# Optimization experiments

Hardware: AMD Instinct MI355X
Metric: run time of the kernel (lower is better)

The kernel has to match this reference:

```python
import jax, jax.numpy as jnp
import numpy as np

N_NODES = 50000
N_EDGES = 800000
N_GRAPHS = 256
F_IN = 128
H = 64
N_CLASSES = 10


def setup_inputs() -> dict:
    key = jax.random.key(0)
    ks = jax.random.split(key, 12)
    x = jax.random.normal(ks[0], (N_NODES, F_IN), dtype=jnp.float32)
    edge_index = jax.random.randint(ks[1], (2, N_EDGES), 0, N_NODES, dtype=jnp.int64)
    batch = jnp.sort(jax.random.randint(ks[2], (N_NODES,), 0, N_GRAPHS, dtype=jnp.int64))
    def glorot(k, fan_in, fan_out):
        lim = np.sqrt(6.0 / (fan_in + fan_out)).astype(np.float32)
        return jax.random.uniform(k, (fan_in, fan_out), jnp.float32, -lim, lim)
    return {
        "x": x,
        "edge_index": edge_index,
        "batch": batch,
        "W1": glorot(ks[3], F_IN, H), "b1": jnp.zeros((H,), jnp.float32),
        "W2": glorot(ks[4], H, H),    "b2": jnp.zeros((H,), jnp.float32),
        "W3": glorot(ks[5], H, H),    "b3": jnp.zeros((H,), jnp.float32),
        "Wm": glorot(ks[6], H, N_CLASSES), "bm": jnp.zeros((N_CLASSES,), jnp.float32),
    }


def _gcn_norm(edge_index, n_nodes):
    # Add self-loops, unit edge weights, symmetric normalization (PyG gcn_norm).
    loops = jnp.arange(n_nodes, dtype=edge_index.dtype)
    row = jnp.concatenate([edge_index[0], loops])  # source
    col = jnp.concatenate([edge_index[1], loops])  # target (aggregation index)
    deg = jax.ops.segment_sum(jnp.ones_like(col, dtype=jnp.float32), col,
                              num_segments=n_nodes)
    dinv = jnp.where(deg > 0, jax.lax.rsqrt(deg), 0.0)
    norm = dinv[row] * dinv[col]  # [E + N]
    return row, col, norm


def _gcn_conv(x, row, col, norm, W, b, n_nodes):
    h = x @ W                                   # [N, H] dense transform
    msg = h[row] * norm[:, None]                # gather + scale  [E+N, H]
    out = jax.ops.segment_sum(msg, col, num_segments=n_nodes)  # scatter-add
    return out + b


def _l2_normalize(x, eps=1e-12):
    n = jnp.sqrt(jnp.sum(x * x, axis=-1, keepdims=True))
    return x / jnp.maximum(n, eps)


def reference(x, edge_index, batch, W1, b1, W2, b2, W3, b3, Wm, bm):
    n = x.shape[0]
    row, col, norm = _gcn_norm(edge_index, n)
    h = x
    for (W, b) in ((W1, b1), (W2, b2), (W3, b3)):
        h = _gcn_conv(h, row, col, norm, W, b, n)
        h = _l2_normalize(h)       # emb_normalize
        h = jax.nn.relu(h)         # gnn_non_linear
    node_emb = h
    # global_mean_pool over graphs
    sums = jax.ops.segment_sum(h, batch, num_segments=N_GRAPHS)
    counts = jax.ops.segment_sum(jnp.ones((n,), jnp.float32), batch,
                                 num_segments=N_GRAPHS)
    graph_emb = sums / jnp.maximum(counts, 1.0)[:, None]
    logits = graph_emb @ Wm + bm
    probs = jax.nn.softmax(logits, axis=-1)
    return logits, probs, node_emb, graph_emb
```

## Files before the change

### kernel.cpp

```cpp
#include <hip/hip_runtime.h>
#include <math.h>

#define HH 64


__global__ void k_init(int* __restrict__ head, float* __restrict__ sums,
                       int* __restrict__ cursor, int n, int pn) {
    int i = blockIdx.x * blockDim.x + threadIdx.x;
    if (i < n) head[i] = -1;
    if (i < pn) sums[i] = 0.f;
    if (i == 0) *cursor = 0;
}

template<int FIN>
__global__ __launch_bounds__(256, 4) void k_link_gemm(const int* __restrict__ col, int E,
                                                      int* __restrict__ head, int* __restrict__ next,
                                                      const float* __restrict__ x,
                                                      const float* __restrict__ W,
                                                      float* __restrict__ lin, int n) {
    constexpr int KC = 32;
    constexpr int XS = 68;
    __shared__ __align__(16) float Ws[FIN][HH];
    __shared__ __align__(16) float xs_t[KC][XS];
    const int tid = threadIdx.x;

    int e0 = blockIdx.x * 1024 + tid;
#pragma unroll
    for (int k = 0; k < 4; ++k) {
        int e = e0 + k * 256;
        if (e < E) {
            int c = col[e];
            int prev = atomicExch(&head[c], e);
            next[e] = prev;
        }
    }

    const int tx = tid & 15;
    const int ty = tid >> 4;
    const int node0 = blockIdx.x * 64;
    if (node0 >= n) return;

    for (int i = tid * 4; i < FIN * HH; i += 1024)
        *(float4*)&Ws[0][i] = *(const float4*)&W[i];

    float acc[4][4] = {};
    const int rr0 = tid >> 3;
    const int cc  = (tid & 7) * 4;

    for (int kc = 0; kc < FIN; kc += KC) {
        __syncthreads();
        for (int rr = rr0; rr < 64; rr += 32) {
            float4 v = make_float4(0.f, 0.f, 0.f, 0.f);
            if (node0 + rr < n) v = *(const float4*)&x[(size_t)(node0 + rr) * FIN + kc + cc];
            xs_t[cc + 0][rr] = v.x;
            xs_t[cc + 1][rr] = v.y;
            xs_t[cc + 2][rr] = v.z;
            xs_t[cc + 3][rr] = v.w;
        }
        __syncthreads();
#pragma unroll 4
        for (int k = 0; k < KC; ++k) {
            float4 a4 = *(const float4*)&xs_t[k][ty * 4];
            float4 b4 = *(const float4*)&Ws[kc + k][tx * 4];
            acc[0][0] = fmaf(a4.x, b4.x, acc[0][0]);
            acc[0][1] = fmaf(a4.x, b4.y, acc[0][1]);
            acc[0][2] = fmaf(a4.x, b4.z, acc[0][2]);
            acc[0][3] = fmaf(a4.x, b4.w, acc[0][3]);
            acc[1][0] = fmaf(a4.y, b4.x, acc[1][0]);
            acc[1][1] = fmaf(a4.y, b4.y, acc[1][1]);
            acc[1][2] = fmaf(a4.y, b4.z, acc[1][2]);
            acc[1][3] = fmaf(a4.y, b4.w, acc[1][3]);
            acc[2][0] = fmaf(a4.z, b4.x, acc[2][0]);
            acc[2][1] = fmaf(a4.z, b4.y, acc[2][1]);
            acc[2][2] = fmaf(a4.z, b4.z, acc[2][2]);
            acc[2][3] = fmaf(a4.z, b4.w, acc[2][3]);
            acc[3][0] = fmaf(a4.w, b4.x, acc[3][0]);
            acc[3][1] = fmaf(a4.w, b4.y, acc[3][1]);
            acc[3][2] = fmaf(a4.w, b4.z, acc[3][2]);
            acc[3][3] = fmaf(a4.w, b4.w, acc[3][3]);
        }
    }

#pragma unroll
    for (int i = 0; i < 4; ++i) {
        int node = node0 + ty * 4 + i;
        if (node < n) *(float4*)&lin[(size_t)node * HH + tx * 4] = *(float4*)acc[i];
    }
}

__global__ __launch_bounds__(256) void k_walk_alloc(const int* __restrict__ row,
                                                    const int* __restrict__ head,
                                                    const int* __restrict__ next,
                                                    int* __restrict__ cursor,
                                                    int* __restrict__ rowptr,
                                                    int* __restrict__ cnt,
                                                    float* __restrict__ dinv,
                                                    int* __restrict__ csr, int n) {
    int node = blockIdx.x * blockDim.x + threadIdx.x;
    int lane = threadIdx.x & 63;
    int len = 0;
    int h = -1;
    if (node < n) {
        h = head[node];
        for (int p = h; p >= 0; p = next[p]) ++len;
        dinv[node] = rsqrtf((float)(len + 1));
    }
    int incl = len;
#pragma unroll
    for (int off = 1; off < 64; off <<= 1) {
        int t = __shfl_up(incl, off, 64);
        if (lane >= off) incl += t;
    }
    int total = __shfl(incl, 63, 64);
    int base = 0;
    if (lane == 0 && total > 0) base = atomicAdd(cursor, total);
    base = __shfl(base, 0, 64);
    int dst = base + incl - len;
    if (node < n) {
        rowptr[node] = dst;
        cnt[node]    = len;
        for (int p = h; p >= 0; p = next[p]) csr[dst++] = row[p];
    }
}

template<int FIN>
__global__ __launch_bounds__(256, 4) void k_gemm2(const float* __restrict__ x,
                                                  const float* __restrict__ W,
                                                  const float* __restrict__ dinv,
                                                  float* __restrict__ linS, int n) {
    constexpr int KC = 32;
    constexpr int XS = 68;
    __shared__ __align__(16) float Ws[FIN][HH];
    __shared__ __align__(16) float xs_t[KC][XS];
    const int tid = threadIdx.x;
    const int tx = tid & 15;
    const int ty = tid >> 4;
    const int node0 = blockIdx.x * 64;

    for (int i = tid * 4; i < FIN * HH; i += 1024)
        *(float4*)&Ws[0][i] = *(const float4*)&W[i];

    float acc[4][4] = {};
    const int rr0 = tid >> 3;
    const int cc  = (tid & 7) * 4;

    for (int kc = 0; kc < FIN; kc += KC) {
        __syncthreads();
        for (int rr = rr0; rr < 64; rr += 32) {
            float4 v = make_float4(0.f, 0.f, 0.f, 0.f);
            if (node0 + rr < n) v = *(const float4*)&x[(size_t)(node0 + rr) * FIN + kc + cc];
            xs_t[cc + 0][rr] = v.x;
            xs_t[cc + 1][rr] = v.y;
            xs_t[cc + 2][rr] = v.z;
            xs_t[cc + 3][rr] = v.w;
        }
        __syncthreads();
#pragma unroll 4
        for (int k = 0; k < KC; ++k) {
            float4 a4 = *(const float4*)&xs_t[k][ty * 4];
            float4 b4 = *(const float4*)&Ws[kc + k][tx * 4];
            acc[0][0] = fmaf(a4.x, b4.x, acc[0][0]);
            acc[0][1] = fmaf(a4.x, b4.y, acc[0][1]);
            acc[0][2] = fmaf(a4.x, b4.z, acc[0][2]);
            acc[0][3] = fmaf(a4.x, b4.w, acc[0][3]);
            acc[1][0] = fmaf(a4.y, b4.x, acc[1][0]);
            acc[1][1] = fmaf(a4.y, b4.y, acc[1][1]);
            acc[1][2] = fmaf(a4.y, b4.z, acc[1][2]);
            acc[1][3] = fmaf(a4.y, b4.w, acc[1][3]);
            acc[2][0] = fmaf(a4.z, b4.x, acc[2][0]);
            acc[2][1] = fmaf(a4.z, b4.y, acc[2][1]);
            acc[2][2] = fmaf(a4.z, b4.z, acc[2][2]);
            acc[2][3] = fmaf(a4.z, b4.w, acc[2][3]);
            acc[3][0] = fmaf(a4.w, b4.x, acc[3][0]);
            acc[3][1] = fmaf(a4.w, b4.y, acc[3][1]);
            acc[3][2] = fmaf(a4.w, b4.z, acc[3][2]);
            acc[3][3] = fmaf(a4.w, b4.w, acc[3][3]);
        }
    }

#pragma unroll
    for (int i = 0; i < 4; ++i) {
        int node = node0 + ty * 4 + i;
        if (node < n) {
            float d = dinv[node];
            float4 o = make_float4(acc[i][0] * d, acc[i][1] * d, acc[i][2] * d, acc[i][3] * d);
            *(float4*)&linS[(size_t)node * HH + tx * 4] = o;
        }
    }
}

__global__ void k_gather_w(const float* __restrict__ lin, const int* __restrict__ csr,
                           const int* __restrict__ rowptr, const int* __restrict__ cnt,
                           const float* __restrict__ dinv, const float* __restrict__ b,
                           float* __restrict__ hout, int n) {
    int node = blockIdx.x * (blockDim.x >> 6) + (threadIdx.x >> 6);
    int lane = threadIdx.x & 63;
    if (node >= n) return;
    int start = rowptr[node];
    int end = start + cnt[node];
    float di = dinv[node];
    float acc0 = di * lin[(size_t)node * HH + lane];
    float acc1 = 0.f, acc2 = 0.f, acc3 = 0.f;
    for (int base = start; base < end; base += 64) {
        int m = end - base; if (m > 64) m = 64;
        int   sv = (base + lane < end) ? csr[base + lane] : 0;
        float wv = (base + lane < end) ? dinv[sv] : 0.f;
        int j = 0;
        for (; j + 3 < m; j += 4) {
            int s0 = __shfl(sv, j, 64);     float w0 = __shfl(wv, j, 64);
            int s1 = __shfl(sv, j + 1, 64); float w1 = __shfl(wv, j + 1, 64);
            int s2 = __shfl(sv, j + 2, 64); float w2 = __shfl(wv, j + 2, 64);
            int s3 = __shfl(sv, j + 3, 64); float w3 = __shfl(wv, j + 3, 64);
            float v0 = lin[(size_t)s0 * HH + lane];
            float v1 = lin[(size_t)s1 * HH + lane];
            float v2 = lin[(size_t)s2 * HH + lane];
            float v3 = lin[(size_t)s3 * HH + lane];
            acc0 = fmaf(w0, v0, acc0);
            acc1 = fmaf(w1, v1, acc1);
            acc2 = fmaf(w2, v2, acc2);
            acc3 = fmaf(w3, v3, acc3);
        }
        for (; j < m; ++j) {
            int s0 = __shfl(sv, j, 64); float w0 = __shfl(wv, j, 64);
            acc0 = fmaf(w0, lin[(size_t)s0 * HH + lane], acc0);
        }
    }
    float v = di * ((acc0 + acc1) + (acc2 + acc3)) + b[lane];
    float ss = v * v;
#pragma unroll
    for (int off = 1; off < 64; off <<= 1) ss += __shfl_xor(ss, off, 64);
    v = v / fmaxf(sqrtf(ss), 1e-12f);
    hout[(size_t)node * HH + lane] = fmaxf(v, 0.f);
}

__global__ void k_gather(const float* __restrict__ linS, const int* __restrict__ csr,
                         const int* __restrict__ rowptr, const int* __restrict__ cnt,
                         const float* __restrict__ dinv, const float* __restrict__ b,
                         float* __restrict__ hout, int n) {
    int node = blockIdx.x * (blockDim.x >> 6) + (threadIdx.x >> 6);
    int lane = threadIdx.x & 63;
    if (node >= n) return;
    int start = rowptr[node];
    int end = start + cnt[node];
    float di = dinv[node];
    float acc0 = linS[(size_t)node * HH + lane];
    float acc1 = 0.f, acc2 = 0.f, acc3 = 0.f;
    for (int base = start; base < end; base += 64) {
        int m = end - base; if (m > 64) m = 64;
        int sv = (base + lane < end) ? csr[base + lane] : 0;
        int j = 0;
        for (; j + 7 < m; j += 8) {
            int s0 = __shfl(sv, j, 64);
            int s1 = __shfl(sv, j + 1, 64);
            int s2 = __shfl(sv, j + 2, 64);
            int s3 = __shfl(sv, j + 3, 64);
            int s4 = __shfl(sv, j + 4, 64);
            int s5 = __shfl(sv, j + 5, 64);
            int s6 = __shfl(sv, j + 6, 64);
            int s7 = __shfl(sv, j + 7, 64);
            float v0 = linS[(size_t)s0 * HH + lane];
            float v1 = linS[(size_t)s1 * HH + lane];
            float v2 = linS[(size_t)s2 * HH + lane];
            float v3 = linS[(size_t)s3 * HH + lane];
            float v4 = linS[(size_t)s4 * HH + lane];
            float v5 = linS[(size_t)s5 * HH + lane];
            float v6 = linS[(size_t)s6 * HH + lane];
            float v7 = linS[(size_t)s7 * HH + lane];
            acc0 += v0; acc1 += v1; acc2 += v2; acc3 += v3;
            acc0 += v4; acc1 += v5; acc2 += v6; acc3 += v7;
        }
        for (; j < m; ++j) {
            int s0 = __shfl(sv, j, 64);
            acc0 += linS[(size_t)s0 * HH + lane];
        }
    }
    float v = di * ((acc0 + acc1) + (acc2 + acc3)) + b[lane];
    float ss = v * v;
#pragma unroll
    for (int off = 1; off < 64; off <<= 1) ss += __shfl_xor(ss, off, 64);
    v = v / fmaxf(sqrtf(ss), 1e-12f);
    hout[(size_t)node * HH + lane] = fmaxf(v, 0.f);
}

__global__ __launch_bounds__(256) void k_pool(const float* __restrict__ node_emb,
                                              const int* __restrict__ batch,
                                              float* __restrict__ sums,
                                              float* __restrict__ cnts, int n) {
    const int NPW = 16;
    int wave = blockIdx.x * 4 + (threadIdx.x >> 6);
    int lane = threadIdx.x & 63;
    int start = wave * NPW;
    if (start >= n) return;
    int end = start + NPW; if (end > n) end = n;
    int cur = batch[start];
    float acc = 0.f;
    int runlen = 0;
    for (int node = start; node < end; ++node) {
        int g = batch[node];
        if (g != cur) {
            atomicAdd(&sums[(size_t)cur * HH + lane], acc);
            if (lane == 0) atomicAdd(&cnts[cur], (float)runlen);
            acc = 0.f; runlen = 0; cur = g;
        }
        acc += node_emb[(size_t)node * HH + lane];
        ++runlen;
    }
    atomicAdd(&sums[(size_t)cur * HH + lane], acc);
    if (lane == 0) atomicAdd(&cnts[cur], (float)runlen);
}

__global__ void k_final2(const float* __restrict__ sums, const float* __restrict__ cnts,
                         const float* __restrict__ Wm, const float* __restrict__ bm,
                         float* __restrict__ logits, float* __restrict__ probs,
                         float* __restrict__ graph_emb) {
    int g = blockIdx.x;
    int lane = threadIdx.x;
    float mean = sums[(size_t)g * HH + lane] / fmaxf(cnts[g], 1.0f);
    graph_emb[(size_t)g * HH + lane] = mean;

    __shared__ float semb[HH];
    __shared__ float slog[16];
    semb[lane] = mean;
    __syncthreads();
    if (lane < 10) {
        float acc = bm[lane];
        for (int k = 0; k < HH; ++k) acc = fmaf(semb[k], Wm[k * 10 + lane], acc);
        slog[lane] = acc;
    }
    __syncthreads();
    if (lane < 10) {
        float mx = -1e30f;
        for (int j = 0; j < 10; ++j) mx = fmaxf(mx, slog[j]);
        float den = 0.f;
        for (int j = 0; j < 10; ++j) den += __expf(slog[j] - mx);
        float lg = slog[lane];
        logits[g * 10 + lane] = lg;
        probs[g * 10 + lane] = __expf(lg - mx) / den;
    }
}


extern "C" void kernel_launch(void* const* d_in, const int* in_sizes, int n_in,
                              void* d_out, int out_size, void* d_ws, size_t ws_size,
                              hipStream_t stream) {
    const float* x     = (const float*)d_in[0];
    const int*   ei    = (const int*)  d_in[1];
    const int*   batch = (const int*)  d_in[2];
    const float* W1 = (const float*)d_in[3];  const float* b1 = (const float*)d_in[4];
    const float* W2 = (const float*)d_in[5];  const float* b2 = (const float*)d_in[6];
    const float* W3 = (const float*)d_in[7];  const float* b3 = (const float*)d_in[8];
    const float* Wm = (const float*)d_in[9];  const float* bm = (const float*)d_in[10];

    const int N = in_sizes[2];
    const int E = in_sizes[1] / 2;
    const int G = (out_size - N * HH) / (2 * 10 + HH);

    const int* row = ei;
    const int* col = ei + E;

    float* out       = (float*)d_out;
    float* logits    = out;
    float* probs     = out + (size_t)G * 10;
    float* node_emb  = out + (size_t)2 * G * 10;
    float* graph_emb = node_emb + (size_t)N * HH;

    char* w = (char*)d_ws;
    auto alloc = [&](size_t bytes) { char* p = w; w += (bytes + 255) & ~(size_t)255; return p; };
    float* dinv    = (float*)alloc((size_t)N * 4);
    int*   cnt     = (int*)  alloc((size_t)N * 4);
    int*   rowptr  = (int*)  alloc((size_t)N * 4);
    int*   head    = (int*)  alloc((size_t)N * 4);
    int*   nxt     = (int*)  alloc((size_t)E * 4);
    int*   cursor  = (int*)  alloc(256);
    float* sums    = (float*)alloc((size_t)G * HH * 4 + (size_t)G * 4);
    float* cnts    = sums + (size_t)G * HH;
    int*   csr     = (int*)  alloc((size_t)E * 4);
    float* lin     = (float*)alloc((size_t)N * HH * 4);
    float* hbuf    = (float*)alloc((size_t)N * HH * 4);

    const int B = 256;
    dim3 blk(B);
    int node_blocks = (N + 3) / 4;
    int gemm_blocks = (N + 63) / 64;
    int nB = (N + B - 1) / B;
    int poolN = G * HH + G;
    int pool_blocks = (N + 63) / 64;

    k_init<<<nB, blk, 0, stream>>>(head, sums, cursor, N, poolN);
    k_link_gemm<128><<<gemm_blocks, blk, 0, stream>>>(col, E, head, nxt, x, W1, lin, N);
    k_walk_alloc<<<nB, blk, 0, stream>>>(row, head, nxt, cursor, rowptr, cnt, dinv, csr, N);

    k_gather_w<<<node_blocks, blk, 0, stream>>>(lin, csr, rowptr, cnt, dinv, b1, hbuf, N);
    k_gemm2<64><<<gemm_blocks, blk, 0, stream>>>(hbuf, W2, dinv, lin, N);
    k_gather<<<node_blocks, blk, 0, stream>>>(lin, csr, rowptr, cnt, dinv, b2, hbuf, N);
    k_gemm2<64><<<gemm_blocks, blk, 0, stream>>>(hbuf, W3, dinv, lin, N);
    k_gather<<<node_blocks, blk, 0, stream>>>(lin, csr, rowptr, cnt, dinv, b3, node_emb, N);

    k_pool<<<pool_blocks, blk, 0, stream>>>(node_emb, batch, sums, cnts, N);
    k_final2<<<G, dim3(64), 0, stream>>>(sums, cnts, Wm, bm, logits, probs, graph_emb);
}
```

Before: 331.5 us.

## Fuse linked-list walk and CSR build into the first GEMM kernel

Edge linking moves out of the first GEMM into its own kernel, and the linked-list walk / CSR allocation (degree count, wave scan, cursor atomic, CSR fill) is fused into the first GEMM kernel instead. The aim is to overlap the latency-bound pointer chasing with the dense GEMM work in the same blocks. Occupancy hint drops from 4 to 3 blocks per CU, and the GEMM output buffers are renamed. Each GEMM block covers 256 nodes for the walk but only 64 for the GEMM, so only the first quarter of blocks do walk work, which may leave it imbalanced.

```diff
diff --git a/kernel.cpp b/kernel.cpp
--- a/kernel.cpp
+++ b/kernel.cpp
@@ -12,9 +12,24 @@
     if (i == 0) *cursor = 0;
 }
 
+__global__ void k_link(const int* __restrict__ col, int E,
+                       int* __restrict__ head, int* __restrict__ next) {
+    int e = blockIdx.x * blockDim.x + threadIdx.x;
+    if (e >= E) return;
+    int c = col[e];
+    int prev = atomicExch(&head[c], e);
+    next[e] = prev;
+}
+
 template<int FIN>
-__global__ __launch_bounds__(256, 4) void k_link_gemm(const int* __restrict__ col, int E,
-                                                      int* __restrict__ head, int* __restrict__ next,
+__global__ __launch_bounds__(256, 3) void k_walk_gemm(const int* __restrict__ row,
+                                                      const int* __restrict__ head,
+                                                      const int* __restrict__ next,
+                                                      int* __restrict__ cursor,
+                                                      int* __restrict__ rowptr,
+                                                      int* __restrict__ cnt,
+                                                      float* __restrict__ dinv,
+                                                      int* __restrict__ csr,
                                                       const float* __restrict__ x,
                                                       const float* __restrict__ W,
                                                       float* __restrict__ lin, int n) {
@@ -24,14 +39,32 @@
     __shared__ __align__(16) float xs_t[KC][XS];
     const int tid = threadIdx.x;
 
-    int e0 = blockIdx.x * 1024 + tid;
+    {
+        int node = blockIdx.x * 256 + tid;
+        int lane = tid & 63;
+        if (node - tid < n) {
+            int len = 0, h = -1;
+            if (node < n) {
+                h = head[node];
+                for (int p = h; p >= 0; p = next[p]) ++len;
+                dinv[node] = rsqrtf((float)(len + 1));
+            }
+            int incl = len;
 #pragma unroll
-    for (int k = 0; k < 4; ++k) {
-        int e = e0 + k * 256;
-        if (e < E) {
-            int c = col[e];
-            int prev = atomicExch(&head[c], e);
-            next[e] = prev;
+            for (int off = 1; off < 64; off <<= 1) {
+                int t = __shfl_up(incl, off, 64);
+                if (lane >= off) incl += t;
+            }
+            int total = __shfl(incl, 63, 64);
+            int base = 0;
+            if (lane == 0 && total > 0) base = atomicAdd(cursor, total);
+            base = __shfl(base, 0, 64);
+            int dst = base + incl - len;
+            if (node < n) {
+                rowptr[node] = dst;
+                cnt[node]    = len;
+                for (int p = h; p >= 0; p = next[p]) csr[dst++] = row[p];
+            }
         }
     }
 
@@ -85,41 +118,6 @@
     for (int i = 0; i < 4; ++i) {
         int node = node0 + ty * 4 + i;
         if (node < n) *(float4*)&lin[(size_t)node * HH + tx * 4] = *(float4*)acc[i];
-    }
-}
-
-__global__ __launch_bounds__(256) void k_walk_alloc(const int* __restrict__ row,
-                                                    const int* __restrict__ head,
-                                                    const int* __restrict__ next,
-                                                    int* __restrict__ cursor,
-                                                    int* __restrict__ rowptr,
-                                                    int* __restrict__ cnt,
-                                                    float* __restrict__ dinv,
-                                                    int* __restrict__ csr, int n) {
-    int node = blockIdx.x * blockDim.x + threadIdx.x;
-    int lane = threadIdx.x & 63;
-    int len = 0;
-    int h = -1;
-    if (node < n) {
-        h = head[node];
-        for (int p = h; p >= 0; p = next[p]) ++len;
-        dinv[node] = rsqrtf((float)(len + 1));
-    }
-    int incl = len;
-#pragma unroll
-    for (int off = 1; off < 64; off <<= 1) {
-        int t = __shfl_up(incl, off, 64);
-        if (lane >= off) incl += t;
-    }
-    int total = __shfl(incl, 63, 64);
-    int base = 0;
-    if (lane == 0 && total > 0) base = atomicAdd(cursor, total);
-    base = __shfl(base, 0, 64);
-    int dst = base + incl - len;
-    if (node < n) {
-        rowptr[node] = dst;
-        cnt[node]    = len;
-        for (int p = h; p >= 0; p = next[p]) csr[dst++] = row[p];
     }
 }
 
@@ -375,26 +373,28 @@
     float* sums    = (float*)alloc((size_t)G * HH * 4 + (size_t)G * 4);
     float* cnts    = sums + (size_t)G * HH;
     int*   csr     = (int*)  alloc((size_t)E * 4);
-    float* lin     = (float*)alloc((size_t)N * HH * 4);
-    float* hbuf    = (float*)alloc((size_t)N * HH * 4);
+    float* bufA    = (float*)alloc((size_t)N * HH * 4);
+    float* bufB    = (float*)alloc((size_t)N * HH * 4);
 
     const int B = 256;
     dim3 blk(B);
     int node_blocks = (N + 3) / 4;
     int gemm_blocks = (N + 63) / 64;
     int nB = (N + B - 1) / B;
+    int eB = (E + B - 1) / B;
     int poolN = G * HH + G;
     int pool_blocks = (N + 63) / 64;
 
     k_init<<<nB, blk, 0, stream>>>(head, sums, cursor, N, poolN);
-    k_link_gemm<128><<<gemm_blocks, blk, 0, stream>>>(col, E, head, nxt, x, W1, lin, N);
-    k_walk_alloc<<<nB, blk, 0, stream>>>(row, head, nxt, cursor, rowptr, cnt, dinv, csr, N);
-
-    k_gather_w<<<node_blocks, blk, 0, stream>>>(lin, csr, rowptr, cnt, dinv, b1, hbuf, N);
-    k_gemm2<64><<<gemm_blocks, blk, 0, stream>>>(hbuf, W2, dinv, lin, N);
-    k_gather<<<node_blocks, blk, 0, stream>>>(lin, csr, rowptr, cnt, dinv, b2, hbuf, N);
-    k_gemm2<64><<<gemm_blocks, blk, 0, stream>>>(hbuf, W3, dinv, lin, N);
-    k_gather<<<node_blocks, blk, 0, stream>>>(lin, csr, rowptr, cnt, dinv, b3, node_emb, N);
+    k_link<<<eB, blk, 0, stream>>>(col, E, head, nxt);
+    k_walk_gemm<128><<<gemm_blocks, blk, 0, stream>>>(row, head, nxt, cursor, rowptr, cnt,
+                                                      dinv, csr, x, W1, bufA, N);
+
+    k_gather_w<<<node_blocks, blk, 0, stream>>>(bufA, csr, rowptr, cnt, dinv, b1, bufB, N);
+    k_gemm2<64><<<gemm_blocks, blk, 0, stream>>>(bufB, W2, dinv, bufA, N);
+    k_gather<<<node_blocks, blk, 0, stream>>>(bufA, csr, rowptr, cnt, dinv, b2, bufB, N);
+    k_gemm2<64><<<gemm_blocks, blk, 0, stream>>>(bufB, W3, dinv, bufA, N);
+    k_gather<<<node_blocks, blk, 0, stream>>>(bufA, csr, rowptr, cnt, dinv, b3, node_emb, N);
 
     k_pool<<<pool_blocks, blk, 0, stream>>>(node_emb, batch, sums, cnts, N);
     k_final2<<<G, dim3(64), 0, stream>>>(sums, cnts, Wm, bm, logits, probs, graph_emb);
```

Result: faster. 321.8 us (-2.9%).
